# Kernel optimization log

Measured on AMD Instinct MI355X. Metric: run time of the kernel, lower is better.

## Reference

```python
import jax, jax.numpy as jnp
import numpy as np
import math

B, S, U, H = 8, 1024, 1024, 16
DK = U // H  # 64


def setup_inputs() -> dict:
    key = jax.random.key(0)
    ks = jax.random.split(key, 12)
    query = jax.random.normal(ks[0], (B, S, U), jnp.float32)
    key_t = jax.random.normal(ks[1], (B, S, U), jnp.float32)  # unused by module (bug preserved)
    value = jax.random.normal(ks[2], (B, S, U), jnp.float32)  # unused by module (bug preserved)
    # causal multiplicative 0/1 mask [B,S,S]
    mask = jnp.broadcast_to(jnp.tril(jnp.ones((S, S), jnp.float32)), (B, S, S))
    bh = math.sqrt(1.0 / DK)   # init bound for per-head projections (out_features=d_k)
    bo = math.sqrt(1.0 / U)    # init bound for output projection (out_features=n_units)
    u = lambda k, shape, b: jax.random.uniform(k, shape, jnp.float32, -b, b)
    # per-head weights stacked: [H, U, DK] (already input->output layout)
    Wq = u(ks[3], (H, U, DK), bh); bq = u(ks[4], (H, DK), bh)
    Wk = u(ks[5], (H, U, DK), bh); bk = u(ks[6], (H, DK), bh)
    Wv = u(ks[7], (H, U, DK), bh); bv = u(ks[8], (H, DK), bh)
    Wo = u(ks[9], (U, U), bo);     bo_ = u(ks[10], (U,), bo)
    return dict(query=query, key=key_t, value=value, mask=mask,
                Wq=Wq, bq=bq, Wk=Wk, bk=bk, Wv=Wv, bv=bv, Wo=Wo, bo=bo_)


def reference(query, key, value, mask, Wq, bq, Wk, bk, Wv, bv, Wo, bo):
    # NOTE: faithful to source — q, k, v are ALL projected from `query`.
    q = jnp.einsum('bsu,hud->bhsd', query, Wq) + bq[:, None, :]
    k = jnp.einsum('bsu,hud->bhsd', query, Wk) + bk[:, None, :]
    v = jnp.einsum('bsu,hud->bhsd', query, Wv) + bv[:, None, :]
    scores = jnp.einsum('bhqd,bhkd->bhqk', q, k) / math.sqrt(DK)
    s = mask[:, None, :, :]  # broadcast over heads
    x = scores * s - 1e9 * (1.0 - s)  # multiplicative mask baked into softmax input
    attn = jax.nn.softmax(x, axis=-1)
    out = jnp.einsum('bhqk,bhkd->bhqd', attn, v)
    # concat heads along feature dim (head 0 first, matching torch.cat order)
    out = out.transpose(0, 2, 1, 3).reshape(B, S, U)
    return out @ Wo + bo
```

## Files before the change

kernel.cpp:

```cpp
#include <hip/hip_runtime.h>
#include <hip/hip_bf16.h>

#define B_ 8
#define S_ 1024
#define U_ 1024
#define H_ 16
#define DK_ 64

typedef __attribute__((ext_vector_type(8))) short short8;
typedef __attribute__((ext_vector_type(4))) float f32x4;
typedef __attribute__((ext_vector_type(16))) float f32x16;

__device__ inline ushort f2b(float x) {
  union { float f; unsigned u; } v; v.f = x;
  unsigned r = (v.u + 0x7FFFu + ((v.u >> 16) & 1u)) >> 16;
  return (ushort)r;
}
__device__ inline unsigned pk2(float lo, float hi) {
  return (unsigned)f2b(lo) | ((unsigned)f2b(hi) << 16);
}

__device__ inline void gld16(const ushort* g, ushort* l) {
  __builtin_amdgcn_global_load_lds((__attribute__((address_space(1))) void*)(g),
                                   (__attribute__((address_space(3))) void*)(l),
                                   16, 0, 0);
}

__global__ __launch_bounds__(256) void pack_x_kern(const float* __restrict__ X,
                                                   ushort* __restrict__ Xb) {
  int idx = blockIdx.x * 256 + threadIdx.x;
  const float4* src = (const float4*)X + (size_t)idx * 2;
  float4 a = src[0], b = src[1];
  ushort r[8];
  r[0]=f2b(a.x); r[1]=f2b(a.y); r[2]=f2b(a.z); r[3]=f2b(a.w);
  r[4]=f2b(b.x); r[5]=f2b(b.y); r[6]=f2b(b.z); r[7]=f2b(b.w);
  *(uint4*)(Xb + (size_t)idx*8) = *(uint4*)r;
}

__global__ __launch_bounds__(256) void pack_w_kern(
    const float* __restrict__ Wq, const float* __restrict__ Wk, const float* __restrict__ Wv,
    const float* __restrict__ bq, const float* __restrict__ bk, const float* __restrict__ bv,
    const float* __restrict__ Wo,
    ushort* __restrict__ Wqkv, float* __restrict__ Bqkv, ushort* __restrict__ Wob)
{
  __shared__ ushort tile[64*65];
  const int t = threadIdx.x;
  const int bid = blockIdx.x;
  if (bid < 768) {
    int p = bid >> 8, rem = bid & 255;
    int h = rem >> 4, kc = rem & 15, k0 = kc*64;
    const float* Wsrc = (p==0) ? Wq : ((p==1) ? Wk : Wv);
    #pragma unroll
    for (int i = 0; i < 16; ++i) {
      int e = t + i*256;
      int r = e >> 6, d = e & 63;
      tile[d*65 + r] = f2b(Wsrc[h*65536 + (k0+r)*64 + d]);
    }
    __syncthreads();
    #pragma unroll
    for (int i = 0; i < 16; ++i) {
      int e = t + i*256;
      int d = e >> 6, r = e & 63;
      Wqkv[(size_t)(p*1024 + h*64 + d)*1024 + k0 + r] = tile[d*65 + r];
    }
    if (kc == 0 && t < 64) {
      const float* bsrc = (p==0) ? bq : ((p==1) ? bk : bv);
      Bqkv[p*1024 + h*64 + t] = bsrc[h*64 + t];
    }
  } else {
    int b2 = bid - 768;
    int nc = b2 >> 4, kc = b2 & 15;
    int n0 = nc*64, k0 = kc*64;
    #pragma unroll
    for (int i = 0; i < 16; ++i) {
      int e = t + i*256;
      int r = e >> 6, d = e & 63;
      tile[d*65 + r] = f2b(Wo[(size_t)(k0+r)*1024 + n0 + d]);
    }
    __syncthreads();
    #pragma unroll
    for (int i = 0; i < 16; ++i) {
      int e = t + i*256;
      int d = e >> 6, r = e & 63;
      Wob[(size_t)(n0+d)*1024 + k0 + r] = tile[d*65 + r];
    }
  }
}

template<int MODE>
__global__ __launch_bounds__(256, 4) void gemm128_kern(
    const ushort* __restrict__ A,
    const ushort* __restrict__ Bw,
    const float* __restrict__ bias,
    ushort* __restrict__ Qb, ushort* __restrict__ Kb, ushort* __restrict__ Vtb,
    float* __restrict__ outF)
{
  __shared__ __align__(16) ushort As[2][4096];
  __shared__ __align__(16) ushort Bs[2][4096];

  const int t = threadIdx.x;
  const int l = t & 63, w = t >> 6;
  const int wr = w >> 1, wc = w & 1;
  const int li = l & 15, c4 = l >> 4;

  int m0, n0;
  if (MODE==0) {
    int swz = (blockIdx.x & 7) * 192 + (blockIdx.x >> 3);
    int ms = swz / 192, rem = swz % 192;
    m0 = (ms*8 + (rem & 7)) * 128;  n0 = (rem >> 3) * 128;
  } else {
    int swz = (blockIdx.x & 7) * 64 + (blockIdx.x >> 3);
    int ms = swz / 64, rem = swz % 64;
    m0 = (ms*8 + (rem & 7)) * 128;  n0 = (rem >> 3) * 128;
  }

  f32x4 acc[4][4];
  #pragma unroll
  for (int i=0;i<4;i++)
    #pragma unroll
    for (int j=0;j<4;j++) acc[i][j] = (f32x4)0.0f;

  auto SA = [&](int buf, int kk) {
    #pragma unroll
    for (int p2=0;p2<2;++p2) {
      int n = p2*256 + t;
      int row = n >> 2, jj = (n & 3) ^ ((row >> 1) & 3);
      gld16(&A[(size_t)(m0 + row)*1024 + kk + jj*8], &As[buf][n*8]);
    }
  };
  auto SB = [&](int buf, int kk) {
    #pragma unroll
    for (int p2=0;p2<2;++p2) {
      int n = p2*256 + t;
      int row = n >> 2, jj = (n & 3) ^ ((row >> 1) & 3);
      gld16(&Bw[(size_t)(n0 + row)*1024 + kk + jj*8], &Bs[buf][n*8]);
    }
  };

  SA(0, 0);  SB(0, 0);
  SA(1, 32); SB(1, 32);

  for (int kt = 0; kt < 32; ++kt) {
    const int cur = kt & 1;
    asm volatile("s_waitcnt vmcnt(4)" ::: "memory");
    __builtin_amdgcn_s_barrier();
    __builtin_amdgcn_sched_barrier(0);

    short8 af[4], bf[4];
    #pragma unroll
    for (int i=0;i<4;i++) {
      int rA = wr*64 + i*16 + li;
      int rB = wc*64 + i*16 + li;
      af[i] = *(const short8*)&As[cur][rA*32 + ((c4 ^ ((rA>>1)&3))*8)];
      bf[i] = *(const short8*)&Bs[cur][rB*32 + ((c4 ^ ((rB>>1)&3))*8)];
    }
    __builtin_amdgcn_s_setprio(1);
    #pragma unroll
    for (int i=0;i<4;i++)
      #pragma unroll
      for (int j=0;j<4;j++)
        acc[i][j] = __builtin_amdgcn_mfma_f32_16x16x32_bf16(af[i], bf[j], acc[i][j], 0,0,0);
    __builtin_amdgcn_s_setprio(0);

    __builtin_amdgcn_s_barrier();
    __builtin_amdgcn_sched_barrier(0);
    const int kk2 = ((kt + 2) & 31) * 32;
    SA(cur, kk2); SB(cur, kk2);
  }

  #pragma unroll
  for (int i=0;i<4;i++) {
    int rbase = m0 + wr*64 + i*16 + c4*4;
    #pragma unroll
    for (int j=0;j<4;j++) {
      int col = n0 + wc*64 + j*16 + li;
      float bv = bias[col];
      if (MODE == 0) {
        int p = col >> 10, h = (col >> 6) & 15, d = col & 63;
        int b = rbase >> 10, s = rbase & 1023;
        if (p == 2) {
          ushort pk4[4];
          #pragma unroll
          for (int r=0;r<4;r++) pk4[r] = f2b(acc[i][j][r] + bv);
          *(uint2*)&Vtb[((size_t)((b*16+h)*64 + d))*1024 + s] = *(uint2*)pk4;
        } else {
          ushort* dst = (p==0) ? Qb : Kb;
          float sc = (p==0) ? 0.18033688011112042f : 1.0f;
          #pragma unroll
          for (int r=0;r<4;r++)
            dst[(((size_t)(b*16 + h))*1024 + s + r)*64 + d] = f2b((acc[i][j][r] + bv) * sc);
        }
      } else {
        #pragma unroll
        for (int r=0;r<4;r++)
          outF[(size_t)(rbase+r)*1024 + col] = acc[i][j][r] + bv;
      }
    }
  }
}

__global__ __launch_bounds__(256, 2) void attn_kern(
    const ushort* __restrict__ Qb, const ushort* __restrict__ Kb,
    const ushort* __restrict__ Vt, ushort* __restrict__ Ob)
{
  __shared__ __align__(16) ushort Pb[4][32*40];
  __shared__ __align__(16) ushort OT[4][32*72];
  const int t = threadIdx.x, l = t & 63, w = t >> 6;
  const int bid = blockIdx.x;
  const int x = bid & 7, i0 = bid >> 3;
  const int bh = x*16 + (i0 >> 2);
  const int p  = (i0 & 3)*4 + w;
  const int qta = p, qtb = 31 - p;

  const int col = l & 31, hi = l >> 5;
  const ushort* Qp = Qb + (size_t)bh*65536;
  const ushort* Kp = Kb + (size_t)bh*65536;
  const ushort* Vp = Vt + (size_t)bh*65536;

  short8 qfa[4], qfb[4];
  #pragma unroll
  for (int m=0;m<4;m++) {
    qfa[m] = *(const short8*)&Qp[(size_t)(qta*32+col)*64 + m*16 + hi*8];
    qfb[m] = *(const short8*)&Qp[(size_t)(qtb*32+col)*64 + m*16 + hi*8];
  }

  f32x16 aA0 = (f32x16)0.0f, aA1 = (f32x16)0.0f;
  f32x16 aB0 = (f32x16)0.0f, aB1 = (f32x16)0.0f;
  float mA = -1e30f, lA = 0.0f, mB = -1e30f, lB = 0.0f;
  ushort* Pw = &Pb[w][0];

  auto PROC = [&](f32x16& s, bool diag, float& mR, float& lS,
                  f32x16& o0, f32x16& o1, const short8* vf0, const short8* vf1) {
    if (diag) {
      #pragma unroll
      for (int r=0;r<16;r++) {
        int kvl = (r&3) + ((r>>2)<<3) + 4*hi;
        s[r] = (kvl > col) ? -1e9f : s[r];
      }
    }
    float mx = s[0];
    #pragma unroll
    for (int r=1;r<16;r++) mx = fmaxf(mx, s[r]);
    mx = fmaxf(mx, __shfl_xor(mx, 32));
    if (__any(mx - mR > 8.0f)) {
      float mN = fmaxf(mR, mx);
      float corr = __builtin_amdgcn_exp2f(mR - mN);
      mR = mN; lS *= corr;
      #pragma unroll
      for (int r=0;r<16;r++) { o0[r] *= corr; o1[r] *= corr; }
    }
    float pr[16], rs = 0.0f;
    #pragma unroll
    for (int r=0;r<16;r++) { pr[r] = __builtin_amdgcn_exp2f(s[r] - mR); rs += pr[r]; }
    rs += __shfl_xor(rs, 32);
    lS += rs;
    #pragma unroll
    for (int r2=0;r2<8;r2++) {
      int r = 2*r2;
      int kv = (r&3) + ((r>>2)<<3) + 4*hi;
      *(unsigned*)&Pw[col*40 + kv] = pk2(pr[r], pr[r+1]);
    }
    short8 pb0 = *(const short8*)&Pw[col*40 + hi*8];
    short8 pb1 = *(const short8*)&Pw[col*40 + 16 + hi*8];
    o0 = __builtin_amdgcn_mfma_f32_32x32x16_bf16(vf0[0], pb0, o0, 0,0,0);
    o0 = __builtin_amdgcn_mfma_f32_32x32x16_bf16(vf0[1], pb1, o0, 0,0,0);
    o1 = __builtin_amdgcn_mfma_f32_32x32x16_bf16(vf1[0], pb0, o1, 0,0,0);
    o1 = __builtin_amdgcn_mfma_f32_32x32x16_bf16(vf1[1], pb1, o1, 0,0,0);
  };

  for (int kt = 0; kt <= qtb; ++kt) {
    short8 kf[4], vf0[2], vf1[2];
    #pragma unroll
    for (int m=0;m<4;m++)
      kf[m] = *(const short8*)&Kp[(size_t)(kt*32+col)*64 + m*16 + hi*8];
    #pragma unroll
    for (int m=0;m<2;m++) {
      vf0[m] = *(const short8*)&Vp[(size_t)col*1024      + kt*32 + m*16 + hi*8];
      vf1[m] = *(const short8*)&Vp[(size_t)(32+col)*1024 + kt*32 + m*16 + hi*8];
    }

    f32x16 sB = (f32x16)0.0f;
    #pragma unroll
    for (int m=0;m<4;m++)
      sB = __builtin_amdgcn_mfma_f32_32x32x16_bf16(kf[m], qfb[m], sB, 0, 0, 0);
    PROC(sB, kt == qtb, mB, lB, aB0, aB1, vf0, vf1);

    if (kt <= qta) {
      f32x16 sA = (f32x16)0.0f;
      #pragma unroll
      for (int m=0;m<4;m++)
        sA = __builtin_amdgcn_mfma_f32_32x32x16_bf16(kf[m], qfa[m], sA, 0, 0, 0);
      PROC(sA, kt == qta, mA, lA, aA0, aA1, vf0, vf1);
    }
  }

  const int b = bh >> 4, h = bh & 15;
  auto EPI = [&](int qt, float lS, const f32x16& o0, const f32x16& o1) {
    float inv = 1.0f / lS;
    ushort* o = &OT[w][0];
    #pragma unroll
    for (int r2=0;r2<8;r2++) {
      int r = 2*r2;
      int dv = (r&3) + ((r>>2)<<3) + 4*hi;
      *(unsigned*)&o[col*72 + dv]      = pk2(o0[r]*inv, o0[r+1]*inv);
      *(unsigned*)&o[col*72 + 32 + dv] = pk2(o1[r]*inv, o1[r+1]*inv);
    }
    #pragma unroll
    for (int it=0; it<4; ++it) {
      int q = it*8 + (l>>3), c8 = (l&7)*8;
      uint4 v = *(const uint4*)&o[q*72 + c8];
      int qg = qt*32 + q;
      *(uint4*)&Ob[(size_t)(b*1024+qg)*1024 + h*64 + c8] = v;
    }
  };
  EPI(qta, lA, aA0, aA1);
  EPI(qtb, lB, aB0, aB1);
}

extern "C" void kernel_launch(void* const* d_in, const int* in_sizes, int n_in,
                              void* d_out, int out_size, void* d_ws, size_t ws_size,
                              hipStream_t stream) {
  const float* query = (const float*)d_in[0];
  const float* Wq = (const float*)d_in[4];
  const float* bq = (const float*)d_in[5];
  const float* Wk = (const float*)d_in[6];
  const float* bk = (const float*)d_in[7];
  const float* Wv = (const float*)d_in[8];
  const float* bv = (const float*)d_in[9];
  const float* Wo = (const float*)d_in[10];
  const float* bo = (const float*)d_in[11];

  char* wsb = (char*)d_ws;
  ushort* Xb   = (ushort*)(wsb);
  ushort* Wqkv = (ushort*)(wsb + 16777216);
  float*  Bqkv = (float*) (wsb + 23068672);
  ushort* Wob  = (ushort*)(wsb + 23080960);
  ushort* Qb   = (ushort*)(wsb + 25178112);
  ushort* Kb   = (ushort*)(wsb + 41955328);
  ushort* Vtb  = (ushort*)(wsb + 58732544);
  ushort* Ob   = (ushort*)(wsb + 75509760);

  hipLaunchKernelGGL(pack_x_kern, dim3(4096), dim3(256), 0, stream, query, Xb);
  hipLaunchKernelGGL(pack_w_kern, dim3(1024), dim3(256), 0, stream,
                     Wq, Wk, Wv, bq, bk, bv, Wo, Wqkv, Bqkv, Wob);
  hipLaunchKernelGGL(gemm128_kern<0>, dim3(1536), dim3(256), 0, stream,
                     Xb, Wqkv, Bqkv, Qb, Kb, Vtb, (float*)nullptr);
  hipLaunchKernelGGL(attn_kern, dim3(512), dim3(256), 0, stream, Qb, Kb, Vtb, Ob);
  hipLaunchKernelGGL(gemm128_kern<1>, dim3(512), dim3(256), 0, stream,
                     Ob, Wob, bo, (ushort*)nullptr, (ushort*)nullptr, (ushort*)nullptr,
                     (float*)d_out);
}
```

Before: 167.8 us.

## Merge pack kernels, triple-buffer GEMM LDS, prefetch K/V in attention

The X and weight pack kernels become one launch, saving a kernel boundary. The GEMM moves from double to triple LDS buffering so the next tile's global-to-LDS load can be issued before the MFMAs, with occupancy lowered from 4 to 3 blocks. The attention kernel software-prefetches the next K/V fragments into registers and interleaves the two query tiles' score MFMAs. This adds register and LDS pressure, and the vmcnt(4) wait with a prefetch distance of two needs its correctness re-checked under the new buffer rotation.

```diff
diff --git a/kernel.cpp b/kernel.cpp
--- a/kernel.cpp
+++ b/kernel.cpp
@@ -26,18 +26,8 @@
                                    16, 0, 0);
 }
 
-__global__ __launch_bounds__(256) void pack_x_kern(const float* __restrict__ X,
-                                                   ushort* __restrict__ Xb) {
-  int idx = blockIdx.x * 256 + threadIdx.x;
-  const float4* src = (const float4*)X + (size_t)idx * 2;
-  float4 a = src[0], b = src[1];
-  ushort r[8];
-  r[0]=f2b(a.x); r[1]=f2b(a.y); r[2]=f2b(a.z); r[3]=f2b(a.w);
-  r[4]=f2b(b.x); r[5]=f2b(b.y); r[6]=f2b(b.z); r[7]=f2b(b.w);
-  *(uint4*)(Xb + (size_t)idx*8) = *(uint4*)r;
-}
-
-__global__ __launch_bounds__(256) void pack_w_kern(
+__global__ __launch_bounds__(256) void pack_all_kern(
+    const float* __restrict__ X, ushort* __restrict__ Xb,
     const float* __restrict__ Wq, const float* __restrict__ Wk, const float* __restrict__ Wv,
     const float* __restrict__ bq, const float* __restrict__ bk, const float* __restrict__ bv,
     const float* __restrict__ Wo,
@@ -45,7 +35,17 @@
 {
   __shared__ ushort tile[64*65];
   const int t = threadIdx.x;
-  const int bid = blockIdx.x;
+  if (blockIdx.x < 4096) {
+    int idx = blockIdx.x * 256 + t;
+    const float4* src = (const float4*)X + (size_t)idx * 2;
+    float4 a = src[0], b = src[1];
+    ushort r[8];
+    r[0]=f2b(a.x); r[1]=f2b(a.y); r[2]=f2b(a.z); r[3]=f2b(a.w);
+    r[4]=f2b(b.x); r[5]=f2b(b.y); r[6]=f2b(b.z); r[7]=f2b(b.w);
+    *(uint4*)(Xb + (size_t)idx*8) = *(uint4*)r;
+    return;
+  }
+  const int bid = blockIdx.x - 4096;
   if (bid < 768) {
     int p = bid >> 8, rem = bid & 255;
     int h = rem >> 4, kc = rem & 15, k0 = kc*64;
@@ -88,15 +88,15 @@
 }
 
 template<int MODE>
-__global__ __launch_bounds__(256, 4) void gemm128_kern(
+__global__ __launch_bounds__(256, 3) void gemm128_kern(
     const ushort* __restrict__ A,
     const ushort* __restrict__ Bw,
     const float* __restrict__ bias,
     ushort* __restrict__ Qb, ushort* __restrict__ Kb, ushort* __restrict__ Vtb,
     float* __restrict__ outF)
 {
-  __shared__ __align__(16) ushort As[2][4096];
-  __shared__ __align__(16) ushort Bs[2][4096];
+  __shared__ __align__(16) ushort As[3][4096];
+  __shared__ __align__(16) ushort Bs[3][4096];
 
   const int t = threadIdx.x;
   const int l = t & 63, w = t >> 6;
@@ -141,7 +141,7 @@
   SA(1, 32); SB(1, 32);
 
   for (int kt = 0; kt < 32; ++kt) {
-    const int cur = kt & 1;
+    const int cur = kt % 3;
     asm volatile("s_waitcnt vmcnt(4)" ::: "memory");
     __builtin_amdgcn_s_barrier();
     __builtin_amdgcn_sched_barrier(0);
@@ -154,6 +154,12 @@
       af[i] = *(const short8*)&As[cur][rA*32 + ((c4 ^ ((rA>>1)&3))*8)];
       bf[i] = *(const short8*)&Bs[cur][rB*32 + ((c4 ^ ((rB>>1)&3))*8)];
     }
+    __builtin_amdgcn_s_barrier();
+    __builtin_amdgcn_sched_barrier(0);
+    const int nb = (kt + 2) % 3;
+    const int kk2 = ((kt + 2) & 31) * 32;
+    SA(nb, kk2); SB(nb, kk2);
+
     __builtin_amdgcn_s_setprio(1);
     #pragma unroll
     for (int i=0;i<4;i++)
@@ -161,11 +167,6 @@
       for (int j=0;j<4;j++)
         acc[i][j] = __builtin_amdgcn_mfma_f32_16x16x32_bf16(af[i], bf[j], acc[i][j], 0,0,0);
     __builtin_amdgcn_s_setprio(0);
-
-    __builtin_amdgcn_s_barrier();
-    __builtin_amdgcn_sched_barrier(0);
-    const int kk2 = ((kt + 2) & 31) * 32;
-    SA(cur, kk2); SB(cur, kk2);
   }
 
   #pragma unroll
@@ -268,30 +269,43 @@
     o1 = __builtin_amdgcn_mfma_f32_32x32x16_bf16(vf1[1], pb1, o1, 0,0,0);
   };
 
+  auto LOADKV = [&](int kt, short8* kf_, short8* v0_, short8* v1_) {
+    #pragma unroll
+    for (int m=0;m<4;m++)
+      kf_[m] = *(const short8*)&Kp[(size_t)(kt*32+col)*64 + m*16 + hi*8];
+    #pragma unroll
+    for (int m=0;m<2;m++) {
+      v0_[m] = *(const short8*)&Vp[(size_t)col*1024      + kt*32 + m*16 + hi*8];
+      v1_[m] = *(const short8*)&Vp[(size_t)(32+col)*1024 + kt*32 + m*16 + hi*8];
+    }
+  };
+
+  short8 kf[4], vf0[2], vf1[2];
+  LOADKV(0, kf, vf0, vf1);
+
   for (int kt = 0; kt <= qtb; ++kt) {
-    short8 kf[4], vf0[2], vf1[2];
-    #pragma unroll
-    for (int m=0;m<4;m++)
-      kf[m] = *(const short8*)&Kp[(size_t)(kt*32+col)*64 + m*16 + hi*8];
-    #pragma unroll
-    for (int m=0;m<2;m++) {
-      vf0[m] = *(const short8*)&Vp[(size_t)col*1024      + kt*32 + m*16 + hi*8];
-      vf1[m] = *(const short8*)&Vp[(size_t)(32+col)*1024 + kt*32 + m*16 + hi*8];
-    }
-
-    f32x16 sB = (f32x16)0.0f;
+    short8 kf2[4], v02[2], v12[2];
+    const int ktn = (kt + 1 <= qtb) ? kt + 1 : qtb;
+    LOADKV(ktn, kf2, v02, v12);
+
+    const bool doA = (kt <= qta);
+    f32x16 sB = (f32x16)0.0f, sA = (f32x16)0.0f;
     #pragma unroll
     for (int m=0;m<4;m++)
       sB = __builtin_amdgcn_mfma_f32_32x32x16_bf16(kf[m], qfb[m], sB, 0, 0, 0);
-    PROC(sB, kt == qtb, mB, lB, aB0, aB1, vf0, vf1);
-
-    if (kt <= qta) {
-      f32x16 sA = (f32x16)0.0f;
+    if (doA) {
       #pragma unroll
       for (int m=0;m<4;m++)
         sA = __builtin_amdgcn_mfma_f32_32x32x16_bf16(kf[m], qfa[m], sA, 0, 0, 0);
-      PROC(sA, kt == qta, mA, lA, aA0, aA1, vf0, vf1);
-    }
+    }
+
+    PROC(sB, kt == qtb, mB, lB, aB0, aB1, vf0, vf1);
+    if (doA) PROC(sA, kt == qta, mA, lA, aA0, aA1, vf0, vf1);
+
+    #pragma unroll
+    for (int m=0;m<4;m++) kf[m] = kf2[m];
+    #pragma unroll
+    for (int m=0;m<2;m++) { vf0[m] = v02[m]; vf1[m] = v12[m]; }
   }
 
   const int b = bh >> 4, h = bh & 15;
@@ -340,9 +354,8 @@
   ushort* Vtb  = (ushort*)(wsb + 58732544);
   ushort* Ob   = (ushort*)(wsb + 75509760);
 
-  hipLaunchKernelGGL(pack_x_kern, dim3(4096), dim3(256), 0, stream, query, Xb);
-  hipLaunchKernelGGL(pack_w_kern, dim3(1024), dim3(256), 0, stream,
-                     Wq, Wk, Wv, bq, bk, bv, Wo, Wqkv, Bqkv, Wob);
+  hipLaunchKernelGGL(pack_all_kern, dim3(5120), dim3(256), 0, stream,
+                     query, Xb, Wq, Wk, Wv, bq, bk, bv, Wo, Wqkv, Bqkv, Wob);
   hipLaunchKernelGGL(gemm128_kern<0>, dim3(1536), dim3(256), 0, stream,
                      Xb, Wqkv, Bqkv, Qb, Kb, Vtb, (float*)nullptr);
   hipLaunchKernelGGL(attn_kern, dim3(512), dim3(256), 0, stream, Qb, Kb, Vtb, Ob);
```

After: 164.4 us. 1.02x faster.
